# Kernel optimization log

Hardware: AMD Instinct MI355X
Metric: run time of the kernel (lower is better)

The kernel has to match this reference:

```python
import jax, jax.numpy as jnp
import numpy as np

# efficient-kan defaults: grid_size=5, spline_order=3, grid_range=[-1, 1]
K_ORDER = 3
GRID_SIZE = 5
NB = GRID_SIZE + K_ORDER  # 8 spline basis functions per input feature
GRID = jnp.arange(-K_ORDER, GRID_SIZE + K_ORDER + 1, dtype=jnp.float32) * (2.0 / GRID_SIZE) - 1.0  # 12 knots on [-2.2, 2.2]


def b_splines(x):
    """Cox-de Boor B-spline basis. x: (..., in) -> (..., in, NB)."""
    g = GRID
    xe = x[..., None]
    bases = ((xe >= g[:-1]) & (xe < g[1:])).astype(x.dtype)
    for p in range(1, K_ORDER + 1):
        bases = ((xe - g[:-(p + 1)]) / (g[p:-1] - g[:-(p + 1)])) * bases[..., :-1] \
              + ((g[p + 1:] - xe) / (g[p + 1:] - g[1:-p])) * bases[..., 1:]
    return bases


def kan_linear(x, base_w, spline_w):
    # base_w: (out, in); spline_w: (out, in, NB)
    base = jnp.einsum('...i,oi->...o', jax.nn.silu(x), base_w)
    spline = jnp.einsum('...ik,oik->...o', b_splines(x), spline_w)
    return base + spline


def kan2(x, b0, s0, b1, s1):
    return kan_linear(kan_linear(x, b0, s0), b1, s1)


def pair_scores(h, b0, s0, b1, s1):
    """All-pairs concat [h_i ; h_j] -> KAN -> scalar score. h: (S, H) -> (S, S)."""
    S, H = h.shape
    q = jnp.broadcast_to(h[:, None, :], (S, S, H))
    k = jnp.broadcast_to(h[None, :, :], (S, S, H))
    pairs = jnp.concatenate([q, k], axis=-1)  # (S, S, 2H)
    return kan2(pairs, b0, s0, b1, s1)[..., 0]  # (S, S)


def setup_inputs() -> dict:
    key = jax.random.key(0)
    ks = jax.random.split(key, 32)
    S, H, KD = 192, 128, 50

    def w(k, shape, scale):
        return jax.random.normal(k, shape, dtype=jnp.float32) * scale

    inp = {
        'x': jax.random.normal(ks[0], (S, H), dtype=jnp.float32),
        'y': jax.random.normal(ks[1], (S, H), dtype=jnp.float32),
        'target': jax.random.normal(ks[2], (S, H), dtype=jnp.float32),
        'bias': w(ks[3], (1,), 0.1),
    }
    # three pairwise-attention KANs: [2H, KD, 1]
    i = 4
    for name in ('xk', 'yk', 'tk'):
        inp[f'{name}_b0'] = w(ks[i + 0], (KD, 2 * H), 0.05)
        inp[f'{name}_s0'] = w(ks[i + 1], (KD, 2 * H, NB), 0.05)
        inp[f'{name}_b1'] = w(ks[i + 2], (1, KD), 0.1)
        inp[f'{name}_s1'] = w(ks[i + 3], (1, KD, NB), 0.1)
        i += 4
    # modal fusion KAN: [3H, KD, 3]
    inp['fk_b0'] = w(ks[i + 0], (KD, 3 * H), 0.05)
    inp['fk_s0'] = w(ks[i + 1], (KD, 3 * H, NB), 0.05)
    inp['fk_b1'] = w(ks[i + 2], (3, KD), 0.1)
    inp['fk_s1'] = w(ks[i + 3], (3, KD, NB), 0.1)
    i += 4
    # output KAN "linears": [H, H]
    inp['l1_b'] = w(ks[i + 0], (H, H), 0.05)
    inp['l1_s'] = w(ks[i + 1], (H, H, NB), 0.05)
    inp['l2_b'] = w(ks[i + 2], (H, H), 0.05)
    inp['l2_s'] = w(ks[i + 3], (H, H, NB), 0.05)
    return inp


def reference(x, y, target, bias,
              xk_b0, xk_s0, xk_b1, xk_s1,
              yk_b0, yk_s0, yk_b1, yk_s1,
              tk_b0, tk_s0, tk_b1, tk_s1,
              fk_b0, fk_s0, fk_b1, fk_s1,
              l1_b, l1_s, l2_b, l2_s):
    # pairwise KAN attention matrices, one per modality (S, S)
    x_att = pair_scores(x, xk_b0, xk_s0, xk_b1, xk_s1)
    y_att = pair_scores(y, yk_b0, yk_s0, yk_b1, yk_s1)
    t_att = pair_scores(target, tk_b0, tk_s0, tk_b1, tk_s1)
    # dynamic modality weights from global mean features
    mf = jnp.concatenate([x.mean(0), y.mean(0), target.mean(0)])[None, :]  # (1, 3H)
    wts = jax.nn.softmax(kan2(mf, fk_b0, fk_s0, fk_b1, fk_s1), axis=-1)[0]  # (3,)
    fusion = wts[0] * x_att + wts[1] * y_att + wts[2] * t_att + bias[0]
    att = jax.nn.softmax(fusion, axis=-1)  # (S, S)
    tgt = att @ target  # (S, H); dropout is identity in eval
    y1 = jax.nn.relu(kan_linear(tgt, l1_b, l1_s))
    y2 = jax.nn.relu(kan_linear(y1, l2_b, l2_s))
    return y2
```

## Files before the change

### kernel.cpp

```cpp
#include <hip/hip_runtime.h>
#include <math.h>

#define SS 192
#define HH 128
#define KDIM 50

#define WT_ELEMS   442368
#define LT_ELEMS   147456
#define FT_ELEMS   221184

__device__ __forceinline__ void kan_phi9(float x, float* o) {
    float g[12];
#pragma unroll
    for (int i = 0; i < 12; ++i) g[i] = (float)(i - 3) * 0.4f - 1.0f;
    float b[11];
#pragma unroll
    for (int i = 0; i < 11; ++i) b[i] = (x >= g[i] && x < g[i + 1]) ? 1.0f : 0.0f;
#pragma unroll
    for (int p = 1; p <= 3; ++p) {
#pragma unroll
        for (int i = 0; i + p < 11; ++i) {
            float l = (x - g[i]) * (1.0f / (g[i + p] - g[i]));
            float r = (g[i + p + 1] - x) * (1.0f / (g[i + p + 1] - g[i + 1]));
            b[i] = l * b[i] + r * b[i + 1];
        }
    }
#pragma unroll
    for (int i = 0; i < 8; ++i) o[i] = b[i];
    o[8] = x / (1.0f + expf(-x));
}

__global__ __launch_bounds__(256) void k0_prep(
    const float* __restrict__ xb0, const float* __restrict__ xs0,
    const float* __restrict__ yb0, const float* __restrict__ ys0,
    const float* __restrict__ tb0, const float* __restrict__ ts0,
    const float* __restrict__ l1b, const float* __restrict__ l1s,
    const float* __restrict__ l2b, const float* __restrict__ l2s,
    const float* __restrict__ fb0, const float* __restrict__ fs0,
    float* __restrict__ wt, float* __restrict__ lt1, float* __restrict__ lt2,
    float* __restrict__ ft)
{
    const int gid = blockIdx.x * 256 + threadIdx.x;
    if (gid < WT_ELEMS) {
        const int kk = gid & 63;
        int t = gid >> 6;
        const int n = t % 9; t /= 9;
        const int h = t & 127; t >>= 7;
        const int half = t & 1;
        const int m = t >> 1;
        const float* b0 = (m == 0) ? xb0 : (m == 1) ? yb0 : tb0;
        const float* s0 = (m == 0) ? xs0 : (m == 1) ? ys0 : ts0;
        float v = 0.f;
        if (kk < KDIM) {
            const int col = half * 128 + h;
            v = (n < 8) ? s0[(kk * 256 + col) * 8 + n] : b0[kk * 256 + col];
        }
        wt[gid] = v;
    } else if (gid < WT_ELEMS + 2 * LT_ELEMS) {
        int idx = gid - WT_ELEMS;
        const int which = idx >= LT_ELEMS;
        if (which) idx -= LT_ELEMS;
        const float* ls = which ? l2s : l1s;
        const float* lb = which ? l2b : l1b;
        const int o = idx & 127;
        const int t = idx >> 7;
        const int n = t % 9;
        const int h = t / 9;
        const float v = (n < 8) ? ls[(o * 128 + h) * 8 + n] : lb[o * 128 + h];
        (which ? lt2 : lt1)[idx] = v;
    } else {
        const int idx = gid - WT_ELEMS - 2 * LT_ELEMS;
        const int kk = idx & 63;
        const int t = idx >> 6;
        const int n = t % 9;
        const int f = t / 9;
        float v = 0.f;
        if (kk < KDIM)
            v = (n < 8) ? fs0[(kk * 384 + f) * 8 + n] : fb0[kk * 384 + f];
        ft[idx] = v;
    }
}

__global__ __launch_bounds__(512) void kf_fusion(
    const float* __restrict__ x, const float* __restrict__ y, const float* __restrict__ tg,
    const float* __restrict__ ft,
    const float* __restrict__ fb1, const float* __restrict__ fs1,
    float* __restrict__ wts)
{
    __shared__ float mfp[768];
    __shared__ float fls[4608];
    __shared__ float zpl[512];
    __shared__ float z[64];
    __shared__ float part3[3 * KDIM];
    const int tid = threadIdx.x;

    for (int idx = tid; idx < 768; idx += 512) {
        const int rh = idx / 384, col = idx % 384;
        const int mm = col >> 7, cc = col & 127;
        const float* in = (mm == 0) ? x : (mm == 1) ? y : tg;
        float s = 0.f;
        for (int r = rh * 96; r < rh * 96 + 96; ++r) s += in[r * HH + cc];
        mfp[col * 2 + rh] = s;
    }
    __syncthreads();
    if (tid < 384) {
        const float v = (mfp[tid * 2] + mfp[tid * 2 + 1]) * (1.0f / 192.0f);
        float ph[9];
        kan_phi9(v, ph);
#pragma unroll
        for (int c = 0; c < 9; ++c) fls[tid * 12 + c] = ph[c];
    }
    __syncthreads();
    {
        const int kk = tid & 63, fs = tid >> 6;
        float a = 0.f;
        for (int f = fs * 48; f < fs * 48 + 48; ++f) {
            const float* ph = fls + f * 12;
            const float* fw = ft + (size_t)f * 9 * 64 + kk;
#pragma unroll
            for (int n = 0; n < 9; ++n) a += ph[n] * fw[n * 64];
        }
        zpl[fs * 64 + kk] = a;
    }
    __syncthreads();
    if (tid < 64) {
        float s = 0.f;
#pragma unroll
        for (int q = 0; q < 8; ++q) s += zpl[q * 64 + tid];
        z[tid] = s;
    }
    __syncthreads();
    if (tid < KDIM) {
        float ph[9];
        kan_phi9(z[tid], ph);
#pragma unroll
        for (int oo = 0; oo < 3; ++oo) {
            float a = ph[8] * fb1[oo * KDIM + tid];
            const float* sw = fs1 + (oo * KDIM + tid) * 8;
#pragma unroll
            for (int n = 0; n < 8; ++n) a += ph[n] * sw[n];
            part3[oo * KDIM + tid] = a;
        }
    }
    __syncthreads();
    if (tid == 0) {
        float o0 = 0.f, o1 = 0.f, o2 = 0.f;
        for (int k = 0; k < KDIM; ++k) {
            o0 += part3[k]; o1 += part3[KDIM + k]; o2 += part3[2 * KDIM + k];
        }
        const float M  = fmaxf(o0, fmaxf(o1, o2));
        const float e0 = expf(o0 - M), e1 = expf(o1 - M), e2 = expf(o2 - M);
        const float s  = e0 + e1 + e2;
        wts[0] = e0 / s; wts[1] = e1 / s; wts[2] = e2 / s;
    }
}

__global__ __launch_bounds__(512) void k1_stage(
    const float* __restrict__ x, const float* __restrict__ y, const float* __restrict__ tg,
    const float* __restrict__ wt,
    float* __restrict__ U, float* __restrict__ Vt)
{
    __shared__ float lds[4096];
    const int tid = threadIdx.x;
    const int m  = blockIdx.x / 96;
    const int i0 = (blockIdx.x % 96) * 2;
    const float* in = (m == 0) ? x : (m == 1) ? y : tg;

    if (tid < 256) {
        const int r = tid >> 7, h = tid & 127;
        float ph[9];
        kan_phi9(in[(i0 + r) * HH + h], ph);
#pragma unroll
        for (int c = 0; c < 9; ++c) lds[r * 1536 + h * 12 + c] = ph[c];
    }
    __syncthreads();

    const int kk   = tid & 63;
    const int half = (tid >> 6) & 1;
    const int hq   = tid >> 7;
    const float* wp = wt + (size_t)(((m * 2 + half) * 128 + hq * 32) * 9) * 64 + kk;
    float a0 = 0.f, a1 = 0.f;
    for (int hl = 0; hl < 32; ++hl) {
        const float* f0 = lds + (hq * 32 + hl) * 12;
        const float* f1 = f0 + 1536;
        const float* wrow = wp + hl * 576;
#pragma unroll
        for (int n = 0; n < 9; ++n) {
            const float w = wrow[n * 64];
            a0 += f0[n] * w; a1 += f1[n] * w;
        }
    }
    float* part = lds + 3072;
    const int pb = ((hq * 2 + half) * 64 + kk) * 2;
    part[pb + 0] = a0; part[pb + 1] = a1;
    __syncthreads();

    if (tid < 128) {
        const int k2 = tid & 63, hf = tid >> 6;
        if (k2 < KDIM) {
#pragma unroll
            for (int r = 0; r < 2; ++r) {
                float s = 0.f;
#pragma unroll
                for (int q = 0; q < 4; ++q) s += part[((q * 2 + hf) * 64 + k2) * 2 + r];
                if (hf == 0) U[(m * SS + i0 + r) * KDIM + k2] = s;
                else         Vt[(m * KDIM + k2) * SS + i0 + r] = s;
            }
        }
    }
}

__global__ __launch_bounds__(576) void k2_att(
    const float* __restrict__ tg,
    const float* __restrict__ xb1, const float* __restrict__ xs1,
    const float* __restrict__ yb1, const float* __restrict__ ys1,
    const float* __restrict__ tb1, const float* __restrict__ ts1,
    const float* __restrict__ bias,
    const float* __restrict__ U, const float* __restrict__ Vt,
    const float* __restrict__ wts, float* __restrict__ out)
{
    __shared__ float spad[3 * KDIM * 14];
    __shared__ float Uls[3 * KDIM];
    __shared__ float b1ls[3 * KDIM];
    __shared__ float smpart[576];
    __shared__ float att[SS];
    __shared__ float opart[512];
    __shared__ float red[20];
    __shared__ float wb[4];
    const int tid = threadIdx.x;
    const int i   = blockIdx.x;
    const int lane = tid & 63, wv = tid >> 6;

    for (int idx = tid; idx < 3 * KDIM * 14; idx += 576) {
        const int m = idx / (KDIM * 14);
        const int r = idx % (KDIM * 14);
        const int k = r / 14, c = r % 14;
        const float* s1 = (m == 0) ? xs1 : (m == 1) ? ys1 : ts1;
        spad[idx] = (c >= 3 && c < 11) ? s1[k * 8 + (c - 3)] : 0.f;
    }
    if (tid < 3 * KDIM) {
        const int m = tid / KDIM, k = tid % KDIM;
        const float* b1 = (m == 0) ? xb1 : (m == 1) ? yb1 : tb1;
        b1ls[tid] = b1[k];
        Uls[tid]  = U[(m * SS + i) * KDIM + k];
    }
    if (tid < 3)  wb[tid] = wts[tid];
    if (tid == 3) wb[3] = bias[0];
    __syncthreads();

    {
        const int m = tid / 192, j = tid % 192;
        const float* vcol = Vt + m * KDIM * SS + j;
        const float* spm  = spad + m * KDIM * 14;
        const float* Um   = Uls + m * KDIM;
        const float* bm   = b1ls + m * KDIM;
        float sm = 0.f;
        for (int k = 0; k < KDIM; ++k) {
            const float zv  = Um[k] + vcol[k * SS];
            const float sig = 1.0f / (1.0f + expf(-zv));
            sm += zv * sig * bm[k];
            float t = (zv + 2.2f) * 2.5f;
            const bool inr = (t >= 0.0f) && (t < 11.0f);
            t = inr ? t : 0.0f;
            const int   c  = (int)t;
            const float u  = t - (float)c;
            const float u2 = u * u, u3 = u2 * u;
            const float wA = (1.0f/6.0f) * (1.0f - 3.0f*u + 3.0f*u2 - u3);
            const float wB = (1.0f/6.0f) * (3.0f*u3 - 6.0f*u2 + 4.0f);
            const float wC = (1.0f/6.0f) * (-3.0f*u3 + 3.0f*u2 + 3.0f*u + 1.0f);
            const float wD = (1.0f/6.0f) * u3;
            const float* sp = spm + k * 14 + c;
            const float spl = wA*sp[0] + wB*sp[1] + wC*sp[2] + wD*sp[3];
            sm += inr ? spl : 0.0f;
        }
        smpart[tid] = wb[m] * sm;
    }
    __syncthreads();

    float f = 0.f;
    if (tid < SS) f = wb[3] + smpart[tid] + smpart[tid + 192] + smpart[tid + 384];
    float mx = f;
#pragma unroll
    for (int o = 32; o > 0; o >>= 1) mx = fmaxf(mx, __shfl_xor(mx, o));
    if (lane == 0) red[wv] = mx;
    __syncthreads();
    mx = fmaxf(red[0], fmaxf(red[1], red[2]));
    const float p = (tid < SS) ? expf(f - mx) : 0.f;
    float sum = p;
#pragma unroll
    for (int o = 32; o > 0; o >>= 1) sum += __shfl_xor(sum, o);
    if (lane == 0) red[10 + wv] = sum;
    __syncthreads();
    sum = red[10] + red[11] + red[12];
    if (tid < SS) att[tid] = p / sum;
    __syncthreads();

    if (tid < 512) {
        const int col = tid & 127, ch = tid >> 7;
        float acc = 0.f;
        for (int jj = ch * 48; jj < ch * 48 + 48; ++jj)
            acc += att[jj] * tg[jj * HH + col];
        opart[tid] = acc;
    }
    __syncthreads();
    if (tid < HH)
        out[i * HH + tid] = opart[tid] + opart[tid + 128] + opart[tid + 256] + opart[tid + 384];
}

__global__ __launch_bounds__(512) void k3_kanlin_relu(
    const float* __restrict__ in, const float* __restrict__ lt,
    float* __restrict__ out)
{
    __shared__ float lds[2048];
    const int tid = threadIdx.x;
    const int i   = blockIdx.x;
    if (tid < 128) {
        float ph[9];
        kan_phi9(in[i * HH + tid], ph);
#pragma unroll
        for (int c = 0; c < 9; ++c) lds[tid * 12 + c] = ph[c];
    }
    __syncthreads();
    const int o  = tid & 127;
    const int hq = tid >> 7;
    const float* wp = lt + (size_t)((hq * 32) * 9) * 128 + o;
    float a = 0.f;
    for (int hl = 0; hl < 32; ++hl) {
        const float* f0 = lds + (hq * 32 + hl) * 12;
        const float* wrow = wp + hl * 1152;
#pragma unroll
        for (int n = 0; n < 9; ++n) a += f0[n] * wrow[n * 128];
    }
    float* part = lds + 1536;
    part[hq * 128 + o] = a;
    __syncthreads();
    if (tid < 128) {
        const float s = part[tid] + part[128 + tid] + part[256 + tid] + part[384 + tid];
        out[i * HH + tid] = fmaxf(s, 0.f);
    }
}

extern "C" void kernel_launch(void* const* d_in, const int* in_sizes, int n_in,
                              void* d_out, int out_size, void* d_ws, size_t ws_size,
                              hipStream_t stream) {
    const float* x    = (const float*)d_in[0];
    const float* y    = (const float*)d_in[1];
    const float* tg   = (const float*)d_in[2];
    const float* bias = (const float*)d_in[3];
    const float* xb0  = (const float*)d_in[4];
    const float* xs0  = (const float*)d_in[5];
    const float* xb1  = (const float*)d_in[6];
    const float* xs1  = (const float*)d_in[7];
    const float* yb0  = (const float*)d_in[8];
    const float* ys0  = (const float*)d_in[9];
    const float* yb1  = (const float*)d_in[10];
    const float* ys1  = (const float*)d_in[11];
    const float* tb0  = (const float*)d_in[12];
    const float* ts0  = (const float*)d_in[13];
    const float* tb1  = (const float*)d_in[14];
    const float* ts1  = (const float*)d_in[15];
    const float* fb0  = (const float*)d_in[16];
    const float* fs0  = (const float*)d_in[17];
    const float* fb1  = (const float*)d_in[18];
    const float* fs1  = (const float*)d_in[19];
    const float* l1b  = (const float*)d_in[20];
    const float* l1s  = (const float*)d_in[21];
    const float* l2b  = (const float*)d_in[22];
    const float* l2s  = (const float*)d_in[23];

    float* ws   = (float*)d_ws;
    float* wt   = ws;
    float* lt1  = wt + WT_ELEMS;
    float* lt2  = lt1 + LT_ELEMS;
    float* ft   = lt2 + LT_ELEMS;
    float* U    = ft + FT_ELEMS;
    float* Vt   = U + 28800;
    float* wts  = Vt + 28800;
    float* tgt  = wts + 64;
    float* y1   = tgt + 24576;
    float* outp = (float*)d_out;

    k0_prep<<<3744, 256, 0, stream>>>(xb0, xs0, yb0, ys0, tb0, ts0,
                                      l1b, l1s, l2b, l2s, fb0, fs0,
                                      wt, lt1, lt2, ft);
    kf_fusion<<<1, 512, 0, stream>>>(x, y, tg, ft, fb1, fs1, wts);
    k1_stage<<<288, 512, 0, stream>>>(x, y, tg, wt, U, Vt);
    k2_att<<<SS, 576, 0, stream>>>(tg, xb1, xs1, yb1, ys1, tb1, ts1, bias,
                                   U, Vt, wts, tgt);
    k3_kanlin_relu<<<192, 512, 0, stream>>>(tgt, lt1, y1);
    k3_kanlin_relu<<<192, 512, 0, stream>>>(y1, lt2, outp);
}
```

Before: 174.3 us.

## Fuse fusion-weight and staging kernels, fold KAN MLP into attention row kernel

The single-block modality-fusion kernel becomes an extra block of the pairwise staging kernel. The two KAN-linear+ReLU layers now run inside the per-row attention kernel, so the row output stays in shared memory instead of going through global intermediates. This cuts the launch count from six to three. The weight-prep kernel now walks the source layout (coalesced reads, scattered writes) and no longer writes the zero padding. Several expf calls become __expf, and the fused row kernel gains shared-memory usage.

```diff
diff --git a/kernel.cpp b/kernel.cpp
--- a/kernel.cpp
+++ b/kernel.cpp
@@ -8,6 +8,10 @@
 #define WT_ELEMS   442368
 #define LT_ELEMS   147456
 #define FT_ELEMS   221184
+
+#define W_SRC      345600
+#define L_SRC      147456
+#define F_SRC      172800
 
 __device__ __forceinline__ void kan_phi9(float x, float* o) {
     float g[12];
@@ -27,7 +31,7 @@
     }
 #pragma unroll
     for (int i = 0; i < 8; ++i) o[i] = b[i];
-    o[8] = x / (1.0f + expf(-x));
+    o[8] = x / (1.0f + __expf(-x));
 }
 
 __global__ __launch_bounds__(256) void k0_prep(
@@ -41,183 +45,173 @@
     float* __restrict__ ft)
 {
     const int gid = blockIdx.x * 256 + threadIdx.x;
-    if (gid < WT_ELEMS) {
-        const int kk = gid & 63;
-        int t = gid >> 6;
-        const int n = t % 9; t /= 9;
-        const int h = t & 127; t >>= 7;
-        const int half = t & 1;
-        const int m = t >> 1;
+    if (gid < W_SRC) {
+        const int n = gid % 9;
+        int t = gid / 9;
+        const int col = t & 255; t >>= 8;
+        const int kk = t % 50;
+        const int m  = t / 50;
         const float* b0 = (m == 0) ? xb0 : (m == 1) ? yb0 : tb0;
         const float* s0 = (m == 0) ? xs0 : (m == 1) ? ys0 : ts0;
-        float v = 0.f;
-        if (kk < KDIM) {
-            const int col = half * 128 + h;
-            v = (n < 8) ? s0[(kk * 256 + col) * 8 + n] : b0[kk * 256 + col];
-        }
-        wt[gid] = v;
-    } else if (gid < WT_ELEMS + 2 * LT_ELEMS) {
-        int idx = gid - WT_ELEMS;
-        const int which = idx >= LT_ELEMS;
-        if (which) idx -= LT_ELEMS;
+        const float v = (n < 8) ? s0[(kk * 256 + col) * 8 + n] : b0[kk * 256 + col];
+        wt[(((m * 2 + (col >> 7)) * 128 + (col & 127)) * 9 + n) * 64 + kk] = v;
+    } else if (gid < W_SRC + 2 * L_SRC) {
+        int idx = gid - W_SRC;
+        const int which = idx >= L_SRC;
+        if (which) idx -= L_SRC;
         const float* ls = which ? l2s : l1s;
         const float* lb = which ? l2b : l1b;
-        const int o = idx & 127;
-        const int t = idx >> 7;
-        const int n = t % 9;
-        const int h = t / 9;
+        const int n = idx % 9;
+        const int t = idx / 9;
+        const int h = t & 127, o = t >> 7;
         const float v = (n < 8) ? ls[(o * 128 + h) * 8 + n] : lb[o * 128 + h];
-        (which ? lt2 : lt1)[idx] = v;
+        (which ? lt2 : lt1)[(h * 9 + n) * 128 + o] = v;
+    } else if (gid < W_SRC + 2 * L_SRC + F_SRC) {
+        const int idx = gid - W_SRC - 2 * L_SRC;
+        const int n = idx % 9;
+        const int t = idx / 9;
+        const int f = t % 384, kk = t / 384;
+        const float v = (n < 8) ? fs0[(kk * 384 + f) * 8 + n] : fb0[kk * 384 + f];
+        ft[(f * 9 + n) * 64 + kk] = v;
+    }
+}
+
+__global__ __launch_bounds__(512) void ka_stage(
+    const float* __restrict__ x, const float* __restrict__ y, const float* __restrict__ tg,
+    const float* __restrict__ wt, const float* __restrict__ ft,
+    const float* __restrict__ fb1, const float* __restrict__ fs1,
+    float* __restrict__ U, float* __restrict__ Vt, float* __restrict__ wts)
+{
+    __shared__ float lds[6144];
+    const int tid = threadIdx.x;
+    const int bid = blockIdx.x;
+
+    if (bid < 288) {
+        const int m  = bid / 96;
+        const int i0 = (bid % 96) * 2;
+        const float* in = (m == 0) ? x : (m == 1) ? y : tg;
+
+        if (tid < 256) {
+            const int r = tid >> 7, h = tid & 127;
+            float ph[9];
+            kan_phi9(in[(i0 + r) * HH + h], ph);
+#pragma unroll
+            for (int c = 0; c < 9; ++c) lds[r * 1536 + h * 12 + c] = ph[c];
+        }
+        __syncthreads();
+
+        const int kk   = tid & 63;
+        const int half = (tid >> 6) & 1;
+        const int hq   = tid >> 7;
+        const float* wp = wt + (size_t)(((m * 2 + half) * 128 + hq * 32) * 9) * 64 + kk;
+        float a0 = 0.f, a1 = 0.f;
+        for (int hl = 0; hl < 32; ++hl) {
+            const float* f0 = lds + (hq * 32 + hl) * 12;
+            const float* f1 = f0 + 1536;
+            const float* wrow = wp + hl * 576;
+#pragma unroll
+            for (int n = 0; n < 9; ++n) {
+                const float w = wrow[n * 64];
+                a0 += f0[n] * w; a1 += f1[n] * w;
+            }
+        }
+        float* part = lds + 3072;
+        const int pb = ((hq * 2 + half) * 64 + kk) * 2;
+        part[pb + 0] = a0; part[pb + 1] = a1;
+        __syncthreads();
+
+        if (tid < 128) {
+            const int k2 = tid & 63, hf = tid >> 6;
+            if (k2 < KDIM) {
+#pragma unroll
+                for (int r = 0; r < 2; ++r) {
+                    float s = 0.f;
+#pragma unroll
+                    for (int q = 0; q < 4; ++q) s += part[((q * 2 + hf) * 64 + k2) * 2 + r];
+                    if (hf == 0) U[(m * SS + i0 + r) * KDIM + k2] = s;
+                    else         Vt[(m * KDIM + k2) * SS + i0 + r] = s;
+                }
+            }
+        }
     } else {
-        const int idx = gid - WT_ELEMS - 2 * LT_ELEMS;
-        const int kk = idx & 63;
-        const int t = idx >> 6;
-        const int n = t % 9;
-        const int f = t / 9;
-        float v = 0.f;
-        if (kk < KDIM)
-            v = (n < 8) ? fs0[(kk * 384 + f) * 8 + n] : fb0[kk * 384 + f];
-        ft[idx] = v;
-    }
-}
-
-__global__ __launch_bounds__(512) void kf_fusion(
-    const float* __restrict__ x, const float* __restrict__ y, const float* __restrict__ tg,
-    const float* __restrict__ ft,
-    const float* __restrict__ fb1, const float* __restrict__ fs1,
-    float* __restrict__ wts)
-{
-    __shared__ float mfp[768];
-    __shared__ float fls[4608];
-    __shared__ float zpl[512];
-    __shared__ float z[64];
-    __shared__ float part3[3 * KDIM];
-    const int tid = threadIdx.x;
-
-    for (int idx = tid; idx < 768; idx += 512) {
-        const int rh = idx / 384, col = idx % 384;
-        const int mm = col >> 7, cc = col & 127;
-        const float* in = (mm == 0) ? x : (mm == 1) ? y : tg;
-        float s = 0.f;
-        for (int r = rh * 96; r < rh * 96 + 96; ++r) s += in[r * HH + cc];
-        mfp[col * 2 + rh] = s;
-    }
-    __syncthreads();
-    if (tid < 384) {
-        const float v = (mfp[tid * 2] + mfp[tid * 2 + 1]) * (1.0f / 192.0f);
-        float ph[9];
-        kan_phi9(v, ph);
-#pragma unroll
-        for (int c = 0; c < 9; ++c) fls[tid * 12 + c] = ph[c];
-    }
-    __syncthreads();
-    {
-        const int kk = tid & 63, fs = tid >> 6;
-        float a = 0.f;
-        for (int f = fs * 48; f < fs * 48 + 48; ++f) {
-            const float* ph = fls + f * 12;
-            const float* fw = ft + (size_t)f * 9 * 64 + kk;
-#pragma unroll
-            for (int n = 0; n < 9; ++n) a += ph[n] * fw[n * 64];
-        }
-        zpl[fs * 64 + kk] = a;
-    }
-    __syncthreads();
-    if (tid < 64) {
-        float s = 0.f;
-#pragma unroll
-        for (int q = 0; q < 8; ++q) s += zpl[q * 64 + tid];
-        z[tid] = s;
-    }
-    __syncthreads();
-    if (tid < KDIM) {
-        float ph[9];
-        kan_phi9(z[tid], ph);
-#pragma unroll
-        for (int oo = 0; oo < 3; ++oo) {
-            float a = ph[8] * fb1[oo * KDIM + tid];
-            const float* sw = fs1 + (oo * KDIM + tid) * 8;
-#pragma unroll
-            for (int n = 0; n < 8; ++n) a += ph[n] * sw[n];
-            part3[oo * KDIM + tid] = a;
-        }
-    }
-    __syncthreads();
-    if (tid == 0) {
-        float o0 = 0.f, o1 = 0.f, o2 = 0.f;
-        for (int k = 0; k < KDIM; ++k) {
-            o0 += part3[k]; o1 += part3[KDIM + k]; o2 += part3[2 * KDIM + k];
-        }
-        const float M  = fmaxf(o0, fmaxf(o1, o2));
-        const float e0 = expf(o0 - M), e1 = expf(o1 - M), e2 = expf(o2 - M);
-        const float s  = e0 + e1 + e2;
-        wts[0] = e0 / s; wts[1] = e1 / s; wts[2] = e2 / s;
-    }
-}
-
-__global__ __launch_bounds__(512) void k1_stage(
-    const float* __restrict__ x, const float* __restrict__ y, const float* __restrict__ tg,
-    const float* __restrict__ wt,
-    float* __restrict__ U, float* __restrict__ Vt)
-{
-    __shared__ float lds[4096];
-    const int tid = threadIdx.x;
-    const int m  = blockIdx.x / 96;
-    const int i0 = (blockIdx.x % 96) * 2;
-    const float* in = (m == 0) ? x : (m == 1) ? y : tg;
-
-    if (tid < 256) {
-        const int r = tid >> 7, h = tid & 127;
-        float ph[9];
-        kan_phi9(in[(i0 + r) * HH + h], ph);
-#pragma unroll
-        for (int c = 0; c < 9; ++c) lds[r * 1536 + h * 12 + c] = ph[c];
-    }
-    __syncthreads();
-
-    const int kk   = tid & 63;
-    const int half = (tid >> 6) & 1;
-    const int hq   = tid >> 7;
-    const float* wp = wt + (size_t)(((m * 2 + half) * 128 + hq * 32) * 9) * 64 + kk;
-    float a0 = 0.f, a1 = 0.f;
-    for (int hl = 0; hl < 32; ++hl) {
-        const float* f0 = lds + (hq * 32 + hl) * 12;
-        const float* f1 = f0 + 1536;
-        const float* wrow = wp + hl * 576;
-#pragma unroll
-        for (int n = 0; n < 9; ++n) {
-            const float w = wrow[n * 64];
-            a0 += f0[n] * w; a1 += f1[n] * w;
-        }
-    }
-    float* part = lds + 3072;
-    const int pb = ((hq * 2 + half) * 64 + kk) * 2;
-    part[pb + 0] = a0; part[pb + 1] = a1;
-    __syncthreads();
-
-    if (tid < 128) {
-        const int k2 = tid & 63, hf = tid >> 6;
-        if (k2 < KDIM) {
-#pragma unroll
-            for (int r = 0; r < 2; ++r) {
-                float s = 0.f;
-#pragma unroll
-                for (int q = 0; q < 4; ++q) s += part[((q * 2 + hf) * 64 + k2) * 2 + r];
-                if (hf == 0) U[(m * SS + i0 + r) * KDIM + k2] = s;
-                else         Vt[(m * KDIM + k2) * SS + i0 + r] = s;
-            }
-        }
-    }
-}
-
-__global__ __launch_bounds__(576) void k2_att(
+        float* mfp   = lds;
+        float* fls   = lds + 768;
+        float* zpl   = lds + 5376;
+        float* z     = lds + 5888;
+        float* part3 = lds + 5952;
+
+        for (int idx = tid; idx < 768; idx += 512) {
+            const int rh = idx / 384, col = idx % 384;
+            const int mm = col >> 7, cc = col & 127;
+            const float* in = (mm == 0) ? x : (mm == 1) ? y : tg;
+            float s = 0.f;
+            for (int r = rh * 96; r < rh * 96 + 96; ++r) s += in[r * HH + cc];
+            mfp[col * 2 + rh] = s;
+        }
+        __syncthreads();
+        if (tid < 384) {
+            const float v = (mfp[tid * 2] + mfp[tid * 2 + 1]) * (1.0f / 192.0f);
+            float ph[9];
+            kan_phi9(v, ph);
+#pragma unroll
+            for (int c = 0; c < 9; ++c) fls[tid * 12 + c] = ph[c];
+        }
+        __syncthreads();
+        {
+            const int kk = tid & 63, fs = tid >> 6;
+            float a = 0.f;
+            for (int f = fs * 48; f < fs * 48 + 48; ++f) {
+                const float* ph = fls + f * 12;
+                const float* fw = ft + (size_t)f * 9 * 64 + kk;
+#pragma unroll
+                for (int n = 0; n < 9; ++n) a += ph[n] * fw[n * 64];
+            }
+            zpl[fs * 64 + kk] = a;
+        }
+        __syncthreads();
+        if (tid < 64) {
+            float s = 0.f;
+#pragma unroll
+            for (int q = 0; q < 8; ++q) s += zpl[q * 64 + tid];
+            z[tid] = s;
+        }
+        __syncthreads();
+        if (tid < KDIM) {
+            float ph[9];
+            kan_phi9(z[tid], ph);
+#pragma unroll
+            for (int oo = 0; oo < 3; ++oo) {
+                float a = ph[8] * fb1[oo * KDIM + tid];
+                const float* sw = fs1 + (oo * KDIM + tid) * 8;
+#pragma unroll
+                for (int n = 0; n < 8; ++n) a += ph[n] * sw[n];
+                part3[oo * KDIM + tid] = a;
+            }
+        }
+        __syncthreads();
+        if (tid == 0) {
+            float o0 = 0.f, o1 = 0.f, o2 = 0.f;
+            for (int k = 0; k < KDIM; ++k) {
+                o0 += part3[k]; o1 += part3[KDIM + k]; o2 += part3[2 * KDIM + k];
+            }
+            const float M  = fmaxf(o0, fmaxf(o1, o2));
+            const float e0 = __expf(o0 - M), e1 = __expf(o1 - M), e2 = __expf(o2 - M);
+            const float s  = e0 + e1 + e2;
+            wts[0] = e0 / s; wts[1] = e1 / s; wts[2] = e2 / s;
+        }
+    }
+}
+
+__global__ __launch_bounds__(576) void kb_row(
     const float* __restrict__ tg,
     const float* __restrict__ xb1, const float* __restrict__ xs1,
     const float* __restrict__ yb1, const float* __restrict__ ys1,
     const float* __restrict__ tb1, const float* __restrict__ ts1,
     const float* __restrict__ bias,
     const float* __restrict__ U, const float* __restrict__ Vt,
-    const float* __restrict__ wts, float* __restrict__ out)
+    const float* __restrict__ wts,
+    const float* __restrict__ lt1, const float* __restrict__ lt2,
+    float* __restrict__ out)
 {
     __shared__ float spad[3 * KDIM * 14];
     __shared__ float Uls[3 * KDIM];
@@ -225,6 +219,9 @@
     __shared__ float smpart[576];
     __shared__ float att[SS];
     __shared__ float opart[512];
+    __shared__ float rowbuf[HH];
+    __shared__ float phi[1536];
+    __shared__ float part[512];
     __shared__ float red[20];
     __shared__ float wb[4];
     const int tid = threadIdx.x;
@@ -257,7 +254,7 @@
         float sm = 0.f;
         for (int k = 0; k < KDIM; ++k) {
             const float zv  = Um[k] + vcol[k * SS];
-            const float sig = 1.0f / (1.0f + expf(-zv));
+            const float sig = 1.0f / (1.0f + __expf(-zv));
             sm += zv * sig * bm[k];
             float t = (zv + 2.2f) * 2.5f;
             const bool inr = (t >= 0.0f) && (t < 11.0f);
@@ -285,7 +282,7 @@
     if (lane == 0) red[wv] = mx;
     __syncthreads();
     mx = fmaxf(red[0], fmaxf(red[1], red[2]));
-    const float p = (tid < SS) ? expf(f - mx) : 0.f;
+    const float p = (tid < SS) ? __expf(f - mx) : 0.f;
     float sum = p;
 #pragma unroll
     for (int o = 32; o > 0; o >>= 1) sum += __shfl_xor(sum, o);
@@ -304,40 +301,40 @@
     }
     __syncthreads();
     if (tid < HH)
-        out[i * HH + tid] = opart[tid] + opart[tid + 128] + opart[tid + 256] + opart[tid + 384];
-}
-
-__global__ __launch_bounds__(512) void k3_kanlin_relu(
-    const float* __restrict__ in, const float* __restrict__ lt,
-    float* __restrict__ out)
-{
-    __shared__ float lds[2048];
-    const int tid = threadIdx.x;
-    const int i   = blockIdx.x;
-    if (tid < 128) {
-        float ph[9];
-        kan_phi9(in[i * HH + tid], ph);
-#pragma unroll
-        for (int c = 0; c < 9; ++c) lds[tid * 12 + c] = ph[c];
-    }
-    __syncthreads();
-    const int o  = tid & 127;
-    const int hq = tid >> 7;
-    const float* wp = lt + (size_t)((hq * 32) * 9) * 128 + o;
-    float a = 0.f;
-    for (int hl = 0; hl < 32; ++hl) {
-        const float* f0 = lds + (hq * 32 + hl) * 12;
-        const float* wrow = wp + hl * 1152;
-#pragma unroll
-        for (int n = 0; n < 9; ++n) a += f0[n] * wrow[n * 128];
-    }
-    float* part = lds + 1536;
-    part[hq * 128 + o] = a;
-    __syncthreads();
-    if (tid < 128) {
-        const float s = part[tid] + part[128 + tid] + part[256 + tid] + part[384 + tid];
-        out[i * HH + tid] = fmaxf(s, 0.f);
-    }
+        rowbuf[tid] = opart[tid] + opart[tid + 128] + opart[tid + 256] + opart[tid + 384];
+    __syncthreads();
+
+#pragma unroll
+    for (int layer = 0; layer < 2; ++layer) {
+        const float* lt = (layer == 0) ? lt1 : lt2;
+        if (tid < HH) {
+            float ph[9];
+            kan_phi9(rowbuf[tid], ph);
+#pragma unroll
+            for (int c = 0; c < 9; ++c) phi[tid * 12 + c] = ph[c];
+        }
+        __syncthreads();
+        if (tid < 512) {
+            const int o  = tid & 127;
+            const int hq = tid >> 7;
+            const float* wp = lt + (size_t)((hq * 32) * 9) * 128 + o;
+            float a = 0.f;
+            for (int hl = 0; hl < 32; ++hl) {
+                const float* f0 = phi + (hq * 32 + hl) * 12;
+                const float* wrow = wp + hl * 1152;
+#pragma unroll
+                for (int n = 0; n < 9; ++n) a += f0[n] * wrow[n * 128];
+            }
+            part[hq * 128 + o] = a;
+        }
+        __syncthreads();
+        if (tid < HH) {
+            const float s = part[tid] + part[128 + tid] + part[256 + tid] + part[384 + tid];
+            rowbuf[tid] = fmaxf(s, 0.f);
+        }
+        __syncthreads();
+    }
+    if (tid < HH) out[i * HH + tid] = rowbuf[tid];
 }
 
 extern "C" void kernel_launch(void* const* d_in, const int* in_sizes, int n_in,
@@ -376,17 +373,12 @@
     float* U    = ft + FT_ELEMS;
     float* Vt   = U + 28800;
     float* wts  = Vt + 28800;
-    float* tgt  = wts + 64;
-    float* y1   = tgt + 24576;
     float* outp = (float*)d_out;
 
-    k0_prep<<<3744, 256, 0, stream>>>(xb0, xs0, yb0, ys0, tb0, ts0,
+    k0_prep<<<3177, 256, 0, stream>>>(xb0, xs0, yb0, ys0, tb0, ts0,
                                       l1b, l1s, l2b, l2s, fb0, fs0,
                                       wt, lt1, lt2, ft);
-    kf_fusion<<<1, 512, 0, stream>>>(x, y, tg, ft, fb1, fs1, wts);
-    k1_stage<<<288, 512, 0, stream>>>(x, y, tg, wt, U, Vt);
-    k2_att<<<SS, 576, 0, stream>>>(tg, xb1, xs1, yb1, ys1, tb1, ts1, bias,
-                                   U, Vt, wts, tgt);
-    k3_kanlin_relu<<<192, 512, 0, stream>>>(tgt, lt1, y1);
-    k3_kanlin_relu<<<192, 512, 0, stream>>>(y1, lt2, outp);
-}
+    ka_stage<<<289, 512, 0, stream>>>(x, y, tg, wt, ft, fb1, fs1, U, Vt, wts);
+    kb_row<<<SS, 576, 0, stream>>>(tg, xb1, xs1, yb1, ys1, tb1, ts1, bias,
+                                   U, Vt, wts, lt1, lt2, outp);
+}
```

After: 162.6 us. 1.07x faster.
